# Optimization experiments

Hardware: AMD Instinct MI355X
Metric: run time of the kernel (lower is better)

Reference implementation:

```python
import jax, jax.numpy as jnp
import numpy as np

DIM, HID, BATCH = 64, 512, 8192


def setup_inputs() -> dict:
    key = jax.random.key(0)
    ks = jax.random.split(key, 6)
    s1 = 1.0 / np.sqrt(DIM + 1)
    s2 = 1.0 / np.sqrt(HID)
    return {
        "t": jax.random.uniform(ks[0], (1,), dtype=jnp.float32),
        "x": jax.random.normal(ks[1], (BATCH, DIM), dtype=jnp.float32),
        "W1": jax.random.normal(ks[2], (DIM + 1, HID), dtype=jnp.float32) * s1,
        "b1": jnp.zeros((HID,), jnp.float32),
        "W2": jax.random.normal(ks[3], (HID, HID), dtype=jnp.float32) * s2,
        "b2": jnp.zeros((HID,), jnp.float32),
        "W3": jax.random.normal(ks[4], (HID, DIM), dtype=jnp.float32) * s2,
        "b3": jnp.zeros((DIM,), jnp.float32),
    }


def _vf_single(ts, xs, W1, b1, W2, b2, W3, b3):
    # xs: [dim], ts: scalar. Time concatenated as extra input feature.
    h = jnp.concatenate([xs, ts[None]])          # [dim+1]
    h = jnp.tanh(h @ W1 + b1)                    # [hid]
    h = jnp.tanh(h @ W2 + b2)                    # [hid]
    return h @ W3 + b3                           # [dim]


def reference(t, x, W1, b1, W2, b2, W3, b3):
    ts = t[0]
    vf = lambda xs: _vf_single(ts, xs, W1, b1, W2, b2, W3, b3)
    v = jax.vmap(vf)(x)                                   # [B, dim]
    # Exact divergence: trace of per-sample Jacobian dv/dx.
    # (Replaces the torch per-dim autograd.grad loop with one batched jacfwd.)
    J = jax.vmap(jax.jacfwd(vf))(x)                       # [B, dim, dim]
    div = jnp.trace(J, axis1=-2, axis2=-1)                # [B]
    return (v, -div[:, None])
```

## Files before the change

### kernel.cpp

```cpp
#include <hip/hip_runtime.h>

#define DIM 64
#define HID 512
#define BATCH 8192
#define MB 32
#define NTHR 512

typedef __attribute__((ext_vector_type(8))) short short8;
typedef __attribute__((ext_vector_type(4))) float f32x4;
typedef __attribute__((ext_vector_type(16))) float f32x16;
typedef float float4_ __attribute__((ext_vector_type(4)));

#define Z16 {0.f,0.f,0.f,0.f,0.f,0.f,0.f,0.f,0.f,0.f,0.f,0.f,0.f,0.f,0.f,0.f}

__device__ __forceinline__ unsigned short f2bf(float f) {
    union { float f; unsigned u; } v; v.f = f;
    return (unsigned short)((v.u + 0x7FFFu + ((v.u >> 16) & 1u)) >> 16);
}
__device__ __forceinline__ float tanh_fast(float x) {
    float e = __expf(2.f * x);
    return 1.f - __fdividef(2.f, e + 1.f);
}

__global__ __launch_bounds__(256) void prep(
        const float* __restrict__ t,  const float* __restrict__ W1,
        const float* __restrict__ b1, const float* __restrict__ W2,
        const float* __restrict__ W3,
        unsigned short* __restrict__ w2pk, unsigned short* __restrict__ ppk,
        unsigned short* __restrict__ w3pk, unsigned short* __restrict__ w1pk,
        float* __restrict__ c1) {
    int b = blockIdx.x;
    if (b >= 288) {
        int n = (b - 288) * 256 + threadIdx.x;
        c1[n] = fmaf(t[0], W1[DIM * HID + n], b1[n]);
        return;
    }
    int gid = b * 256 + threadIdx.x;
    int f = gid >> 6, l = gid & 63;
    if (f < 512) {
        int nt = f >> 5, ks = f & 31;
        int n = nt * 32 + (l & 31), k0 = ks * 16 + (l >> 5) * 8;
        unsigned short* o = w2pk + (size_t)(f * 64 + l) * 8;
#pragma unroll
        for (int e = 0; e < 8; ++e) o[e] = f2bf(W2[(size_t)(k0 + e) * HID + n]);
    } else if (f < 1024) {
        int fi = f - 512;
        int nt = fi >> 5, ks = fi & 31;
        int n = nt * 32 + (l & 31), k0 = ks * 16 + (l >> 5) * 8;
        float m[8] = {0.f,0.f,0.f,0.f,0.f,0.f,0.f,0.f};
        for (int i = 0; i < DIM; ++i) {
            float w3 = W3[(size_t)n * DIM + i];
#pragma unroll
            for (int e = 0; e < 8; ++e) m[e] = fmaf(W1[(size_t)i * HID + k0 + e], w3, m[e]);
        }
        unsigned short* o = ppk + (size_t)(fi * 64 + l) * 8;
#pragma unroll
        for (int e = 0; e < 8; ++e) o[e] = f2bf(W2[(size_t)(k0 + e) * HID + n] * m[e]);
    } else if (f < 1088) {
        int fi = f - 1024;
        int nt = fi >> 4, ks = fi & 15;
        int n = nt * 16 + (l & 15), k0 = ks * 32 + (l >> 4) * 8;
        unsigned short* o = w3pk + (size_t)(fi * 64 + l) * 8;
#pragma unroll
        for (int e = 0; e < 8; ++e) o[e] = f2bf(W3[(size_t)(k0 + e) * DIM + n]);
    } else {
        int fi = f - 1088;
        int nt = fi >> 1, ks = fi & 1;
        int n = nt * 16 + (l & 15), k0 = ks * 32 + (l >> 4) * 8;
        unsigned short* o = w1pk + (size_t)(fi * 64 + l) * 8;
#pragma unroll
        for (int e = 0; e < 8; ++e) o[e] = f2bf(W1[(size_t)(k0 + e) * HID + n]);
    }
}

__device__ __forceinline__ int lds_addr(int row, int k) {
    return (row * 1024 + k * 2) ^ ((row & 7) << 4);
}

__global__ __launch_bounds__(NTHR, 2) void fused_main(
        const float* __restrict__ x,  const float* __restrict__ c1,
        const float* __restrict__ b2, const float* __restrict__ b3,
        const unsigned short* __restrict__ w1pk, const unsigned short* __restrict__ w2pk,
        const unsigned short* __restrict__ ppk,  const unsigned short* __restrict__ w3pk,
        float* __restrict__ out) {
    __shared__ unsigned short h1s[MB * HID];
    __shared__ unsigned short d1s[MB * HID];
    __shared__ unsigned short h2s[MB * HID];
    __shared__ float wred[8][MB];

    const int tid = threadIdx.x;
    const int w = tid >> 6;
    const int l = tid & 63;
    const int lr = l & 15, g = l >> 4;
    const int wm = w & 1, wn = w >> 1;
    const int s0 = blockIdx.x * MB;
    char* h1b = (char*)h1s; char* d1b = (char*)d1s; char* h2b = (char*)h2s;

    union U8 { short8 s8; unsigned short u[8]; };
    short8 ax[2];
#pragma unroll
    for (int ks = 0; ks < 2; ++ks) {
        const float* xp = x + (size_t)(s0 + wm * 16 + lr) * DIM + ks * 32 + g * 8;
        float4_ x0 = *(const float4_*)xp;
        float4_ x1 = *(const float4_*)(xp + 4);
        U8 u;
        u.u[0] = f2bf(x0.x); u.u[1] = f2bf(x0.y); u.u[2] = f2bf(x0.z); u.u[3] = f2bf(x0.w);
        u.u[4] = f2bf(x1.x); u.u[5] = f2bf(x1.y); u.u[6] = f2bf(x1.z); u.u[7] = f2bf(x1.w);
        ax[ks] = u.s8;
    }
    {
        f32x4 acc1[8];
#pragma unroll
        for (int nt = 0; nt < 8; ++nt) {
            const short8* bw = (const short8*)w1pk + (size_t)((wn * 8 + nt) * 2) * 64 + l;
            f32x4 a = {0.f, 0.f, 0.f, 0.f};
            a = __builtin_amdgcn_mfma_f32_16x16x32_bf16(ax[0], bw[0],  a, 0, 0, 0);
            a = __builtin_amdgcn_mfma_f32_16x16x32_bf16(ax[1], bw[64], a, 0, 0, 0);
            acc1[nt] = a;
        }
#pragma unroll
        for (int nt = 0; nt < 8; ++nt) {
            int c = (wn * 8 + nt) * 16 + lr;
            float c1v = c1[c];
#pragma unroll
            for (int r = 0; r < 4; ++r) {
                int row = wm * 16 + g * 4 + r;
                float h = tanh_fast(acc1[nt][r] + c1v);
                int a0 = lds_addr(row, c);
                *(unsigned short*)(h1b + a0) = f2bf(h);
                *(unsigned short*)(d1b + a0) = f2bf(fmaf(-h, h, 1.f));
            }
        }
    }
    __syncthreads();

    const int nt0 = w * 2, nt1 = w * 2 + 1;
    f32x16 z0 = Z16, z1 = Z16, sv0 = Z16, sv1 = Z16;
#pragma unroll 4
    for (int ks = 0; ks < 32; ++ks) {
        int arow = l & 31;
        int ab = lds_addr(arow, ks * 16 + (l >> 5) * 8);
        short8 ah = *(const short8*)(h1b + ab);
        short8 ad = *(const short8*)(d1b + ab);
        const short8* bw = (const short8*)w2pk;
        const short8* bp = (const short8*)ppk;
        short8 bw0 = bw[(size_t)(nt0 * 32 + ks) * 64 + l];
        short8 bw1 = bw[(size_t)(nt1 * 32 + ks) * 64 + l];
        short8 bp0 = bp[(size_t)(nt0 * 32 + ks) * 64 + l];
        short8 bp1 = bp[(size_t)(nt1 * 32 + ks) * 64 + l];
        z0  = __builtin_amdgcn_mfma_f32_32x32x16_bf16(ah, bw0, z0, 0, 0, 0);
        z1  = __builtin_amdgcn_mfma_f32_32x32x16_bf16(ah, bw1, z1, 0, 0, 0);
        sv0 = __builtin_amdgcn_mfma_f32_32x32x16_bf16(ad, bp0, sv0, 0, 0, 0);
        sv1 = __builtin_amdgcn_mfma_f32_32x32x16_bf16(ad, bp1, sv1, 0, 0, 0);
    }

    float divp[16];
#pragma unroll
    for (int r = 0; r < 16; ++r) divp[r] = 0.f;
#pragma unroll
    for (int j = 0; j < 2; ++j) {
        f32x16 z  = j ? z1 : z0;
        f32x16 sv = j ? sv1 : sv0;
        int c = (w * 2 + j) * 32 + (l & 31);
        float b2v = b2[c];
#pragma unroll
        for (int r = 0; r < 16; ++r) {
            int row = (r & 3) + 8 * (r >> 2) + 4 * (l >> 5);
            float h2 = tanh_fast(z[r] + b2v);
            float d2 = fmaf(-h2, h2, 1.f);
            divp[r] = fmaf(sv[r], d2, divp[r]);
            *(unsigned short*)(h2b + lds_addr(row, c)) = f2bf(h2);
        }
    }

#pragma unroll
    for (int off = 1; off < 32; off <<= 1) {
#pragma unroll
        for (int r = 0; r < 16; ++r) divp[r] += __shfl_xor(divp[r], off, 64);
    }
    if ((l & 31) == 0) {
#pragma unroll
        for (int r = 0; r < 16; ++r) {
            int row = (r & 3) + 8 * (r >> 2) + 4 * (l >> 5);
            wred[w][row] = divp[r];
        }
    }
    __syncthreads();
    if (tid < MB) {
        float d = 0.f;
#pragma unroll
        for (int ww = 0; ww < 8; ++ww) d += wred[ww][tid];
        out[(size_t)BATCH * DIM + s0 + tid] = -d;
    }

    {
        f32x4 acc = {0.f, 0.f, 0.f, 0.f};
        const short8* bw = (const short8*)w3pk + (size_t)(wn * 16) * 64 + l;
#pragma unroll
        for (int ks = 0; ks < 16; ++ks) {
            int ab = lds_addr(wm * 16 + lr, ks * 32 + g * 8);
            short8 a2 = *(const short8*)(h2b + ab);
            acc = __builtin_amdgcn_mfma_f32_16x16x32_bf16(a2, bw[ks * 64], acc, 0, 0, 0);
        }
        int c = wn * 16 + lr;
        float b3v = b3[c];
#pragma unroll
        for (int r = 0; r < 4; ++r)
            out[(size_t)(s0 + wm * 16 + g * 4 + r) * DIM + c] = acc[r] + b3v;
    }
}

extern "C" void kernel_launch(void* const* d_in, const int* in_sizes, int n_in,
                              void* d_out, int out_size, void* d_ws, size_t ws_size,
                              hipStream_t stream) {
    const float* t  = (const float*)d_in[0];
    const float* x  = (const float*)d_in[1];
    const float* W1 = (const float*)d_in[2];
    const float* b1 = (const float*)d_in[3];
    const float* W2 = (const float*)d_in[4];
    const float* b2 = (const float*)d_in[5];
    const float* W3 = (const float*)d_in[6];
    const float* b3 = (const float*)d_in[7];
    float* out = (float*)d_out;

    char* ws = (char*)d_ws;
    unsigned short* w2pk = (unsigned short*)ws;
    unsigned short* ppk  = (unsigned short*)(ws + (512 << 10));
    unsigned short* w3pk = (unsigned short*)(ws + (1 << 20));
    unsigned short* w1pk = (unsigned short*)(ws + (1 << 20) + (64 << 10));
    float*          c1   = (float*)(ws + (1 << 20) + (128 << 10));

    prep<<<290, 256, 0, stream>>>(t, W1, b1, W2, W3, w2pk, ppk, w3pk, w1pk, c1);
    fused_main<<<BATCH / MB, NTHR, 0, stream>>>(x, c1, b2, b3, w1pk, w2pk, ppk, w3pk, out);
}
```

Before: 36.95 us.

## Split hidden dimension across block pairs with 64-sample tiles and atomic output accumulation

Each block now processes 64 samples and half of the layer-2 output columns, so the grid doubles and each block streams half of the W2 and P weights. Warps are split into two roles, one computing the W2 product and one the divergence product, and layer-3 partial sums and divergence are combined across the two halves with float atomics into a pre-zeroed output. Prep is adjusted to stage W3 in shared memory and to repack W3 by half. This adds a memset, atomic traffic, larger shared-memory use and a heavier prep block, in exchange for reusing weight loads across more samples.

```diff
diff --git a/kernel.cpp b/kernel.cpp
--- a/kernel.cpp
+++ b/kernel.cpp
@@ -3,19 +3,27 @@
 #define DIM 64
 #define HID 512
 #define BATCH 8192
-#define MB 32
+#define SPB 64
 #define NTHR 512
 
 typedef __attribute__((ext_vector_type(8))) short short8;
 typedef __attribute__((ext_vector_type(4))) float f32x4;
 typedef __attribute__((ext_vector_type(16))) float f32x16;
 typedef float float4_ __attribute__((ext_vector_type(4)));
+typedef unsigned long long ull;
 
 #define Z16 {0.f,0.f,0.f,0.f,0.f,0.f,0.f,0.f,0.f,0.f,0.f,0.f,0.f,0.f,0.f,0.f}
+
+union U8 { short8 s8; unsigned short u[8]; };
+union U4 { ull v; unsigned short u[4]; };
+union FB { unsigned u; float f; };
 
 __device__ __forceinline__ unsigned short f2bf(float f) {
     union { float f; unsigned u; } v; v.f = f;
     return (unsigned short)((v.u + 0x7FFFu + ((v.u >> 16) & 1u)) >> 16);
+}
+__device__ __forceinline__ float bf2f(unsigned short b) {
+    FB v; v.u = (unsigned)b << 16; return v.f;
 }
 __device__ __forceinline__ float tanh_fast(float x) {
     float e = __expf(2.f * x);
@@ -29,6 +37,7 @@
         unsigned short* __restrict__ w2pk, unsigned short* __restrict__ ppk,
         unsigned short* __restrict__ w3pk, unsigned short* __restrict__ w1pk,
         float* __restrict__ c1) {
+    __shared__ float w3sT[DIM * 513];
     int b = blockIdx.x;
     if (b >= 288) {
         int n = (b - 288) * 256 + threadIdx.x;
@@ -44,12 +53,17 @@
 #pragma unroll
         for (int e = 0; e < 8; ++e) o[e] = f2bf(W2[(size_t)(k0 + e) * HID + n]);
     } else if (f < 1024) {
+        for (int idx = threadIdx.x; idx < HID * DIM; idx += 256) {
+            int n = idx >> 6, i = idx & 63;
+            w3sT[i * 513 + n] = W3[idx];
+        }
+        __syncthreads();
         int fi = f - 512;
         int nt = fi >> 5, ks = fi & 31;
         int n = nt * 32 + (l & 31), k0 = ks * 16 + (l >> 5) * 8;
         float m[8] = {0.f,0.f,0.f,0.f,0.f,0.f,0.f,0.f};
         for (int i = 0; i < DIM; ++i) {
-            float w3 = W3[(size_t)n * DIM + i];
+            float w3 = w3sT[i * 513 + n];
 #pragma unroll
             for (int e = 0; e < 8; ++e) m[e] = fmaf(W1[(size_t)i * HID + k0 + e], w3, m[e]);
         }
@@ -58,8 +72,8 @@
         for (int e = 0; e < 8; ++e) o[e] = f2bf(W2[(size_t)(k0 + e) * HID + n] * m[e]);
     } else if (f < 1088) {
         int fi = f - 1024;
-        int nt = fi >> 4, ks = fi & 15;
-        int n = nt * 16 + (l & 15), k0 = ks * 32 + (l >> 4) * 8;
+        int half = fi >> 5, nt = (fi >> 3) & 3, ks = fi & 7;
+        int n = nt * 16 + (l & 15), k0 = half * 256 + ks * 32 + (l >> 4) * 8;
         unsigned short* o = w3pk + (size_t)(fi * 64 + l) * 8;
 #pragma unroll
         for (int e = 0; e < 8; ++e) o[e] = f2bf(W3[(size_t)(k0 + e) * DIM + n]);
@@ -73,140 +87,152 @@
     }
 }
 
-__device__ __forceinline__ int lds_addr(int row, int k) {
-    return (row * 1024 + k * 2) ^ ((row & 7) << 4);
-}
-
 __global__ __launch_bounds__(NTHR, 2) void fused_main(
         const float* __restrict__ x,  const float* __restrict__ c1,
         const float* __restrict__ b2, const float* __restrict__ b3,
         const unsigned short* __restrict__ w1pk, const unsigned short* __restrict__ w2pk,
         const unsigned short* __restrict__ ppk,  const unsigned short* __restrict__ w3pk,
         float* __restrict__ out) {
-    __shared__ unsigned short h1s[MB * HID];
-    __shared__ unsigned short d1s[MB * HID];
-    __shared__ unsigned short h2s[MB * HID];
-    __shared__ float wred[8][MB];
-
-    const int tid = threadIdx.x;
-    const int w = tid >> 6;
-    const int l = tid & 63;
+    __shared__ unsigned short h1s[SPB * HID];
+    __shared__ unsigned short d1s[SPB * HID];
+    char* h1b = (char*)h1s;
+    char* d1b = (char*)d1s;
+
+    const int tid = threadIdx.x, w = tid >> 6, l = tid & 63;
     const int lr = l & 15, g = l >> 4;
-    const int wm = w & 1, wn = w >> 1;
-    const int s0 = blockIdx.x * MB;
-    char* h1b = (char*)h1s; char* d1b = (char*)d1s; char* h2b = (char*)h2s;
-
-    union U8 { short8 s8; unsigned short u[8]; };
-    short8 ax[2];
-#pragma unroll
-    for (int ks = 0; ks < 2; ++ks) {
-        const float* xp = x + (size_t)(s0 + wm * 16 + lr) * DIM + ks * 32 + g * 8;
-        float4_ x0 = *(const float4_*)xp;
-        float4_ x1 = *(const float4_*)(xp + 4);
-        U8 u;
-        u.u[0] = f2bf(x0.x); u.u[1] = f2bf(x0.y); u.u[2] = f2bf(x0.z); u.u[3] = f2bf(x0.w);
-        u.u[4] = f2bf(x1.x); u.u[5] = f2bf(x1.y); u.u[6] = f2bf(x1.z); u.u[7] = f2bf(x1.w);
-        ax[ks] = u.s8;
-    }
-    {
-        f32x4 acc1[8];
-#pragma unroll
-        for (int nt = 0; nt < 8; ++nt) {
-            const short8* bw = (const short8*)w1pk + (size_t)((wn * 8 + nt) * 2) * 64 + l;
-            f32x4 a = {0.f, 0.f, 0.f, 0.f};
-            a = __builtin_amdgcn_mfma_f32_16x16x32_bf16(ax[0], bw[0],  a, 0, 0, 0);
-            a = __builtin_amdgcn_mfma_f32_16x16x32_bf16(ax[1], bw[64], a, 0, 0, 0);
-            acc1[nt] = a;
-        }
-#pragma unroll
-        for (int nt = 0; nt < 8; ++nt) {
-            int c = (wn * 8 + nt) * 16 + lr;
-            float c1v = c1[c];
+    const int s0   = (blockIdx.x >> 1) * SPB;
+    const int half = blockIdx.x & 1;
+
+    short8 xf[4][2];
+#pragma unroll
+    for (int nt = 0; nt < 4; ++nt)
+#pragma unroll
+        for (int ks = 0; ks < 2; ++ks) {
+            const float* xp = x + (size_t)(s0 + nt * 16 + lr) * DIM + ks * 32 + g * 8;
+            float4_ x0 = *(const float4_*)xp;
+            float4_ x1 = *(const float4_*)(xp + 4);
+            U8 u;
+            u.u[0]=f2bf(x0.x); u.u[1]=f2bf(x0.y); u.u[2]=f2bf(x0.z); u.u[3]=f2bf(x0.w);
+            u.u[4]=f2bf(x1.x); u.u[5]=f2bf(x1.y); u.u[6]=f2bf(x1.z); u.u[7]=f2bf(x1.w);
+            xf[nt][ks] = u.s8;
+        }
+#pragma unroll
+    for (int mi = 0; mi < 4; ++mi) {
+        int mt = w * 4 + mi;
+        short8 a0 = ((const short8*)w1pk)[(size_t)((mt * 2 + 0) * 64 + l)];
+        short8 a1 = ((const short8*)w1pk)[(size_t)((mt * 2 + 1) * 64 + l)];
+        float c1q[4];
+#pragma unroll
+        for (int r = 0; r < 4; ++r) c1q[r] = c1[mt * 16 + g * 4 + r];
+#pragma unroll
+        for (int nt = 0; nt < 4; ++nt) {
+            f32x4 acc = {0.f, 0.f, 0.f, 0.f};
+            acc = __builtin_amdgcn_mfma_f32_16x16x32_bf16(a0, xf[nt][0], acc, 0, 0, 0);
+            acc = __builtin_amdgcn_mfma_f32_16x16x32_bf16(a1, xf[nt][1], acc, 0, 0, 0);
+            int sample = nt * 16 + lr;
+            U4 hu, du;
 #pragma unroll
             for (int r = 0; r < 4; ++r) {
-                int row = wm * 16 + g * 4 + r;
-                float h = tanh_fast(acc1[nt][r] + c1v);
-                int a0 = lds_addr(row, c);
-                *(unsigned short*)(h1b + a0) = f2bf(h);
-                *(unsigned short*)(d1b + a0) = f2bf(fmaf(-h, h, 1.f));
+                float h = tanh_fast(acc[r] + c1q[r]);
+                hu.u[r] = f2bf(h);
+                du.u[r] = f2bf(fmaf(-h, h, 1.f));
             }
+            int ab = (sample * 1024 + (mt * 16 + g * 4) * 2) ^ ((sample & 15) << 4);
+            *(ull*)(h1b + ab) = hu.v;
+            *(ull*)(d1b + ab) = du.v;
         }
     }
     __syncthreads();
 
-    const int nt0 = w * 2, nt1 = w * 2 + 1;
-    f32x16 z0 = Z16, z1 = Z16, sv0 = Z16, sv1 = Z16;
+    const int role = w >> 2;
+    const int wp = w & 3;
+    const int mgA = half * 8 + wp * 2, mgB = mgA + 1;
+    const short8* Af = (const short8*)(role ? ppk : w2pk);
+    const char* Bb = role ? d1b : h1b;
+
+    f32x16 a00 = Z16, a01 = Z16, a10 = Z16, a11 = Z16;
 #pragma unroll 4
     for (int ks = 0; ks < 32; ++ks) {
-        int arow = l & 31;
-        int ab = lds_addr(arow, ks * 16 + (l >> 5) * 8);
-        short8 ah = *(const short8*)(h1b + ab);
-        short8 ad = *(const short8*)(d1b + ab);
-        const short8* bw = (const short8*)w2pk;
-        const short8* bp = (const short8*)ppk;
-        short8 bw0 = bw[(size_t)(nt0 * 32 + ks) * 64 + l];
-        short8 bw1 = bw[(size_t)(nt1 * 32 + ks) * 64 + l];
-        short8 bp0 = bp[(size_t)(nt0 * 32 + ks) * 64 + l];
-        short8 bp1 = bp[(size_t)(nt1 * 32 + ks) * 64 + l];
-        z0  = __builtin_amdgcn_mfma_f32_32x32x16_bf16(ah, bw0, z0, 0, 0, 0);
-        z1  = __builtin_amdgcn_mfma_f32_32x32x16_bf16(ah, bw1, z1, 0, 0, 0);
-        sv0 = __builtin_amdgcn_mfma_f32_32x32x16_bf16(ad, bp0, sv0, 0, 0, 0);
-        sv1 = __builtin_amdgcn_mfma_f32_32x32x16_bf16(ad, bp1, sv1, 0, 0, 0);
-    }
-
-    float divp[16];
-#pragma unroll
-    for (int r = 0; r < 16; ++r) divp[r] = 0.f;
-#pragma unroll
-    for (int j = 0; j < 2; ++j) {
-        f32x16 z  = j ? z1 : z0;
-        f32x16 sv = j ? sv1 : sv0;
-        int c = (w * 2 + j) * 32 + (l & 31);
-        float b2v = b2[c];
-#pragma unroll
-        for (int r = 0; r < 16; ++r) {
-            int row = (r & 3) + 8 * (r >> 2) + 4 * (l >> 5);
-            float h2 = tanh_fast(z[r] + b2v);
-            float d2 = fmaf(-h2, h2, 1.f);
-            divp[r] = fmaf(sv[r], d2, divp[r]);
-            *(unsigned short*)(h2b + lds_addr(row, c)) = f2bf(h2);
-        }
-    }
-
-#pragma unroll
-    for (int off = 1; off < 32; off <<= 1) {
-#pragma unroll
-        for (int r = 0; r < 16; ++r) divp[r] += __shfl_xor(divp[r], off, 64);
-    }
-    if ((l & 31) == 0) {
-#pragma unroll
-        for (int r = 0; r < 16; ++r) {
-            int row = (r & 3) + 8 * (r >> 2) + 4 * (l >> 5);
-            wred[w][row] = divp[r];
-        }
+        int cb = ks * 32 + (l >> 5) * 16;
+        int r0 = l & 31, r1 = 32 + (l & 31);
+        short8 b0  = *(const short8*)(Bb + ((r0 * 1024 + cb) ^ ((r0 & 15) << 4)));
+        short8 b1v = *(const short8*)(Bb + ((r1 * 1024 + cb) ^ ((r1 & 15) << 4)));
+        short8 aA = Af[(size_t)((mgA * 32 + ks) * 64 + l)];
+        short8 aB = Af[(size_t)((mgB * 32 + ks) * 64 + l)];
+        a00 = __builtin_amdgcn_mfma_f32_32x32x16_bf16(aA, b0,  a00, 0, 0, 0);
+        a01 = __builtin_amdgcn_mfma_f32_32x32x16_bf16(aA, b1v, a01, 0, 0, 0);
+        a10 = __builtin_amdgcn_mfma_f32_32x32x16_bf16(aB, b0,  a10, 0, 0, 0);
+        a11 = __builtin_amdgcn_mfma_f32_32x32x16_bf16(aB, b1v, a11, 0, 0, 0);
     }
     __syncthreads();
-    if (tid < MB) {
-        float d = 0.f;
-#pragma unroll
-        for (int ww = 0; ww < 8; ++ww) d += wred[ww][tid];
-        out[(size_t)BATCH * DIM + s0 + tid] = -d;
+
+    const int hh = l >> 5;
+    if (role == 0) {
+#define Z_EPI(ACC, J, N2) { \
+        int mloc = wp * 2 + (J); \
+        int cgbase = (half * 8 + mloc) * 32; \
+        int sample = (N2) * 32 + (l & 31); \
+        _Pragma("unroll") \
+        for (int q = 0; q < 4; ++q) { \
+            U4 hu; \
+            _Pragma("unroll") \
+            for (int r3 = 0; r3 < 4; ++r3) { \
+                int rm = r3 + 8 * q + 4 * hh; \
+                float h2 = tanh_fast((ACC)[q * 4 + r3] + b2[cgbase + rm]); \
+                hu.u[r3] = f2bf(h2); \
+            } \
+            int ab = (sample * 512 + (mloc * 32 + 8 * q + 4 * hh) * 2) ^ ((sample & 15) << 4); \
+            *(ull*)(d1b + ab) = hu.v; \
+        } }
+        Z_EPI(a00, 0, 0) Z_EPI(a01, 0, 1) Z_EPI(a10, 1, 0) Z_EPI(a11, 1, 1)
+#undef Z_EPI
+    }
+    __syncthreads();
+    if (role == 1) {
+        float ds0 = 0.f, ds1 = 0.f;
+#define S_EPI(ACC, J, N2, DS) { \
+        int mloc = wp * 2 + (J); \
+        int sample = (N2) * 32 + (l & 31); \
+        _Pragma("unroll") \
+        for (int q = 0; q < 4; ++q) { \
+            int ab = (sample * 512 + (mloc * 32 + 8 * q + 4 * hh) * 2) ^ ((sample & 15) << 4); \
+            U4 hu; hu.v = *(const ull*)(d1b + ab); \
+            _Pragma("unroll") \
+            for (int r3 = 0; r3 < 4; ++r3) { \
+                float h2 = bf2f(hu.u[r3]); \
+                DS = fmaf((ACC)[q * 4 + r3], fmaf(-h2, h2, 1.f), DS); \
+            } \
+        } }
+        S_EPI(a00, 0, 0, ds0) S_EPI(a01, 0, 1, ds1) S_EPI(a10, 1, 0, ds0) S_EPI(a11, 1, 1, ds1)
+#undef S_EPI
+        ds0 += __shfl_xor(ds0, 32, 64);
+        ds1 += __shfl_xor(ds1, 32, 64);
+        if (l < 32) {
+            atomicAdd(out + (size_t)BATCH * DIM + s0 + l,      -ds0);
+            atomicAdd(out + (size_t)BATCH * DIM + s0 + 32 + l, -ds1);
+        }
     }
 
     {
-        f32x4 acc = {0.f, 0.f, 0.f, 0.f};
-        const short8* bw = (const short8*)w3pk + (size_t)(wn * 16) * 64 + l;
-#pragma unroll
-        for (int ks = 0; ks < 16; ++ks) {
-            int ab = lds_addr(wm * 16 + lr, ks * 32 + g * 8);
-            short8 a2 = *(const short8*)(h2b + ab);
-            acc = __builtin_amdgcn_mfma_f32_16x16x32_bf16(a2, bw[ks * 64], acc, 0, 0, 0);
-        }
-        int c = wn * 16 + lr;
-        float b3v = b3[c];
-#pragma unroll
-        for (int r = 0; r < 4; ++r)
-            out[(size_t)(s0 + wm * 16 + g * 4 + r) * DIM + c] = acc[r] + b3v;
+        const int mt3 = w >> 1, ntp = (w & 1) * 2;
+#pragma unroll
+        for (int jj = 0; jj < 2; ++jj) {
+            int nt = ntp + jj;
+            f32x4 acc3 = {0.f, 0.f, 0.f, 0.f};
+            const short8* W3f = (const short8*)w3pk + (size_t)((half * 32 + nt * 8) * 64 + l);
+#pragma unroll
+            for (int ks = 0; ks < 8; ++ks) {
+                int row = mt3 * 16 + lr;
+                int ab = (row * 512 + ks * 64 + g * 16) ^ ((row & 15) << 4);
+                short8 ah = *(const short8*)(d1b + ab);
+                acc3 = __builtin_amdgcn_mfma_f32_16x16x32_bf16(ah, W3f[ks * 64], acc3, 0, 0, 0);
+            }
+            float bv = half ? 0.f : b3[nt * 16 + lr];
+#pragma unroll
+            for (int r = 0; r < 4; ++r)
+                atomicAdd(out + (size_t)(s0 + mt3 * 16 + g * 4 + r) * DIM + nt * 16 + lr,
+                          acc3[r] + bv);
+        }
     }
 }
 
@@ -230,6 +256,7 @@
     unsigned short* w1pk = (unsigned short*)(ws + (1 << 20) + (64 << 10));
     float*          c1   = (float*)(ws + (1 << 20) + (128 << 10));
 
+    hipMemsetAsync(d_out, 0, (size_t)out_size * sizeof(float), stream);
     prep<<<290, 256, 0, stream>>>(t, W1, b1, W2, W3, w2pk, ppk, w3pk, w1pk, c1);
-    fused_main<<<BATCH / MB, NTHR, 0, stream>>>(x, c1, b2, b3, w1pk, w2pk, ppk, w3pk, out);
-}
+    fused_main<<<(BATCH / SPB) * 2, NTHR, 0, stream>>>(x, c1, b2, b3, w1pk, w2pk, ppk, w3pk, out);
+}
```

After: 45.79 us. +23.9%, slower.

## Use 1024-thread blocks with transposed layer-1 MFMA and prefetched layer-2 weights

Applied to the files above, without the earlier changes.

Doubles the block to 16 waves so each wave computes one 32-column tile of the hidden layer instead of two. Layer 1 is recomputed as W1^T times x^T, so each lane writes 4 contiguous bf16 values as one 64-bit LDS store, and the LDS swizzle is widened. The layer-2 loop software-prefetches the next weight fragments. The prep kernel now stages W3 in shared memory for the P-matrix build. The costs are the lost two-blocks-per-CU launch bound and half the waves sitting idle during the layer-3 matmul.

```diff
diff --git a/kernel.cpp b/kernel.cpp
--- a/kernel.cpp
+++ b/kernel.cpp
@@ -4,14 +4,18 @@
 #define HID 512
 #define BATCH 8192
 #define MB 32
-#define NTHR 512
+#define NTHR 1024
 
 typedef __attribute__((ext_vector_type(8))) short short8;
 typedef __attribute__((ext_vector_type(4))) float f32x4;
 typedef __attribute__((ext_vector_type(16))) float f32x16;
 typedef float float4_ __attribute__((ext_vector_type(4)));
+typedef unsigned long long ull;
 
 #define Z16 {0.f,0.f,0.f,0.f,0.f,0.f,0.f,0.f,0.f,0.f,0.f,0.f,0.f,0.f,0.f,0.f}
+
+union U8 { short8 s8; unsigned short u[8]; };
+union U4 { ull v; unsigned short u[4]; };
 
 __device__ __forceinline__ unsigned short f2bf(float f) {
     union { float f; unsigned u; } v; v.f = f;
@@ -29,6 +33,7 @@
         unsigned short* __restrict__ w2pk, unsigned short* __restrict__ ppk,
         unsigned short* __restrict__ w3pk, unsigned short* __restrict__ w1pk,
         float* __restrict__ c1) {
+    __shared__ float w3sT[DIM * 33];
     int b = blockIdx.x;
     if (b >= 288) {
         int n = (b - 288) * 256 + threadIdx.x;
@@ -44,12 +49,19 @@
 #pragma unroll
         for (int e = 0; e < 8; ++e) o[e] = f2bf(W2[(size_t)(k0 + e) * HID + n]);
     } else if (f < 1024) {
+        int ntb = (b * 4 - 512) >> 5;
+        for (int idx = threadIdx.x; idx < 32 * DIM; idx += 256) {
+            int dn = idx >> 6, i = idx & 63;
+            w3sT[i * 33 + dn] = W3[(size_t)(ntb * 32 + dn) * DIM + i];
+        }
+        __syncthreads();
         int fi = f - 512;
-        int nt = fi >> 5, ks = fi & 31;
-        int n = nt * 32 + (l & 31), k0 = ks * 16 + (l >> 5) * 8;
+        int ks = fi & 31;
+        int dn = l & 31, k0 = ks * 16 + (l >> 5) * 8;
+        int n = ntb * 32 + dn;
         float m[8] = {0.f,0.f,0.f,0.f,0.f,0.f,0.f,0.f};
         for (int i = 0; i < DIM; ++i) {
-            float w3 = W3[(size_t)n * DIM + i];
+            float w3 = w3sT[i * 33 + dn];
 #pragma unroll
             for (int e = 0; e < 8; ++e) m[e] = fmaf(W1[(size_t)i * HID + k0 + e], w3, m[e]);
         }
@@ -73,11 +85,11 @@
     }
 }
 
-__device__ __forceinline__ int lds_addr(int row, int k) {
-    return (row * 1024 + k * 2) ^ ((row & 7) << 4);
-}
-
-__global__ __launch_bounds__(NTHR, 2) void fused_main(
+__device__ __forceinline__ int act_addr(int sample, int colbyte) {
+    return (sample * 1024 + colbyte) ^ ((sample & 15) << 4);
+}
+
+__global__ __launch_bounds__(NTHR) void fused_main(
         const float* __restrict__ x,  const float* __restrict__ c1,
         const float* __restrict__ b2, const float* __restrict__ b3,
         const unsigned short* __restrict__ w1pk, const unsigned short* __restrict__ w2pk,
@@ -86,93 +98,83 @@
     __shared__ unsigned short h1s[MB * HID];
     __shared__ unsigned short d1s[MB * HID];
     __shared__ unsigned short h2s[MB * HID];
-    __shared__ float wred[8][MB];
-
-    const int tid = threadIdx.x;
-    const int w = tid >> 6;
-    const int l = tid & 63;
+    __shared__ float wred[16][MB];
+    char* h1b = (char*)h1s; char* d1b = (char*)d1s; char* h2b = (char*)h2s;
+
+    const int tid = threadIdx.x, w = tid >> 6, l = tid & 63;
     const int lr = l & 15, g = l >> 4;
-    const int wm = w & 1, wn = w >> 1;
     const int s0 = blockIdx.x * MB;
-    char* h1b = (char*)h1s; char* d1b = (char*)d1s; char* h2b = (char*)h2s;
-
-    union U8 { short8 s8; unsigned short u[8]; };
-    short8 ax[2];
-#pragma unroll
-    for (int ks = 0; ks < 2; ++ks) {
-        const float* xp = x + (size_t)(s0 + wm * 16 + lr) * DIM + ks * 32 + g * 8;
-        float4_ x0 = *(const float4_*)xp;
-        float4_ x1 = *(const float4_*)(xp + 4);
-        U8 u;
-        u.u[0] = f2bf(x0.x); u.u[1] = f2bf(x0.y); u.u[2] = f2bf(x0.z); u.u[3] = f2bf(x0.w);
-        u.u[4] = f2bf(x1.x); u.u[5] = f2bf(x1.y); u.u[6] = f2bf(x1.z); u.u[7] = f2bf(x1.w);
-        ax[ks] = u.s8;
-    }
-    {
-        f32x4 acc1[8];
-#pragma unroll
-        for (int nt = 0; nt < 8; ++nt) {
-            const short8* bw = (const short8*)w1pk + (size_t)((wn * 8 + nt) * 2) * 64 + l;
-            f32x4 a = {0.f, 0.f, 0.f, 0.f};
-            a = __builtin_amdgcn_mfma_f32_16x16x32_bf16(ax[0], bw[0],  a, 0, 0, 0);
-            a = __builtin_amdgcn_mfma_f32_16x16x32_bf16(ax[1], bw[64], a, 0, 0, 0);
-            acc1[nt] = a;
-        }
-#pragma unroll
-        for (int nt = 0; nt < 8; ++nt) {
-            int c = (wn * 8 + nt) * 16 + lr;
-            float c1v = c1[c];
+
+    short8 xf[2][2];
+#pragma unroll
+    for (int nt = 0; nt < 2; ++nt)
+#pragma unroll
+        for (int ks = 0; ks < 2; ++ks) {
+            const float* xp = x + (size_t)(s0 + nt * 16 + lr) * DIM + ks * 32 + g * 8;
+            float4_ x0 = *(const float4_*)xp;
+            float4_ x1 = *(const float4_*)(xp + 4);
+            U8 u;
+            u.u[0]=f2bf(x0.x); u.u[1]=f2bf(x0.y); u.u[2]=f2bf(x0.z); u.u[3]=f2bf(x0.w);
+            u.u[4]=f2bf(x1.x); u.u[5]=f2bf(x1.y); u.u[6]=f2bf(x1.z); u.u[7]=f2bf(x1.w);
+            xf[nt][ks] = u.s8;
+        }
+#pragma unroll
+    for (int mi = 0; mi < 2; ++mi) {
+        int mt = w * 2 + mi;
+        short8 a0 = ((const short8*)w1pk)[(size_t)((mt * 2 + 0) * 64 + l)];
+        short8 a1 = ((const short8*)w1pk)[(size_t)((mt * 2 + 1) * 64 + l)];
+        float c1q[4];
+#pragma unroll
+        for (int r = 0; r < 4; ++r) c1q[r] = c1[mt * 16 + g * 4 + r];
+#pragma unroll
+        for (int nt = 0; nt < 2; ++nt) {
+            f32x4 acc = {0.f, 0.f, 0.f, 0.f};
+            acc = __builtin_amdgcn_mfma_f32_16x16x32_bf16(a0, xf[nt][0], acc, 0, 0, 0);
+            acc = __builtin_amdgcn_mfma_f32_16x16x32_bf16(a1, xf[nt][1], acc, 0, 0, 0);
+            int sample = nt * 16 + lr;
+            U4 hu, du;
 #pragma unroll
             for (int r = 0; r < 4; ++r) {
-                int row = wm * 16 + g * 4 + r;
-                float h = tanh_fast(acc1[nt][r] + c1v);
-                int a0 = lds_addr(row, c);
-                *(unsigned short*)(h1b + a0) = f2bf(h);
-                *(unsigned short*)(d1b + a0) = f2bf(fmaf(-h, h, 1.f));
+                float h = tanh_fast(acc[r] + c1q[r]);
+                hu.u[r] = f2bf(h);
+                du.u[r] = f2bf(fmaf(-h, h, 1.f));
             }
+            int ab = act_addr(sample, (mt * 16 + g * 4) * 2);
+            *(ull*)(h1b + ab) = hu.v;
+            *(ull*)(d1b + ab) = du.v;
         }
     }
     __syncthreads();
 
-    const int nt0 = w * 2, nt1 = w * 2 + 1;
-    f32x16 z0 = Z16, z1 = Z16, sv0 = Z16, sv1 = Z16;
-#pragma unroll 4
+    const short8* bw = (const short8*)w2pk + (size_t)(w * 32) * 64 + l;
+    const short8* bp = (const short8*)ppk  + (size_t)(w * 32) * 64 + l;
+    f32x16 z = Z16, s = Z16;
+    short8 bwc = bw[0], bpc = bp[0];
+#pragma unroll 8
     for (int ks = 0; ks < 32; ++ks) {
-        int arow = l & 31;
-        int ab = lds_addr(arow, ks * 16 + (l >> 5) * 8);
+        short8 bwn = bwc, bpn = bpc;
+        if (ks < 31) { bwn = bw[(ks + 1) * 64]; bpn = bp[(ks + 1) * 64]; }
+        int ab = act_addr(l & 31, ks * 32 + (l >> 5) * 16);
         short8 ah = *(const short8*)(h1b + ab);
         short8 ad = *(const short8*)(d1b + ab);
-        const short8* bw = (const short8*)w2pk;
-        const short8* bp = (const short8*)ppk;
-        short8 bw0 = bw[(size_t)(nt0 * 32 + ks) * 64 + l];
-        short8 bw1 = bw[(size_t)(nt1 * 32 + ks) * 64 + l];
-        short8 bp0 = bp[(size_t)(nt0 * 32 + ks) * 64 + l];
-        short8 bp1 = bp[(size_t)(nt1 * 32 + ks) * 64 + l];
-        z0  = __builtin_amdgcn_mfma_f32_32x32x16_bf16(ah, bw0, z0, 0, 0, 0);
-        z1  = __builtin_amdgcn_mfma_f32_32x32x16_bf16(ah, bw1, z1, 0, 0, 0);
-        sv0 = __builtin_amdgcn_mfma_f32_32x32x16_bf16(ad, bp0, sv0, 0, 0, 0);
-        sv1 = __builtin_amdgcn_mfma_f32_32x32x16_bf16(ad, bp1, sv1, 0, 0, 0);
+        z = __builtin_amdgcn_mfma_f32_32x32x16_bf16(ah, bwc, z, 0, 0, 0);
+        s = __builtin_amdgcn_mfma_f32_32x32x16_bf16(ad, bpc, s, 0, 0, 0);
+        bwc = bwn; bpc = bpn;
     }
 
     float divp[16];
-#pragma unroll
-    for (int r = 0; r < 16; ++r) divp[r] = 0.f;
-#pragma unroll
-    for (int j = 0; j < 2; ++j) {
-        f32x16 z  = j ? z1 : z0;
-        f32x16 sv = j ? sv1 : sv0;
-        int c = (w * 2 + j) * 32 + (l & 31);
+    {
+        int c = w * 32 + (l & 31);
         float b2v = b2[c];
 #pragma unroll
         for (int r = 0; r < 16; ++r) {
             int row = (r & 3) + 8 * (r >> 2) + 4 * (l >> 5);
             float h2 = tanh_fast(z[r] + b2v);
             float d2 = fmaf(-h2, h2, 1.f);
-            divp[r] = fmaf(sv[r], d2, divp[r]);
-            *(unsigned short*)(h2b + lds_addr(row, c)) = f2bf(h2);
-        }
-    }
-
+            divp[r] = s[r] * d2;
+            *(unsigned short*)(h2b + act_addr(row, c * 2)) = f2bf(h2);
+        }
+    }
 #pragma unroll
     for (int off = 1; off < 32; off <<= 1) {
 #pragma unroll
@@ -189,24 +191,25 @@
     if (tid < MB) {
         float d = 0.f;
 #pragma unroll
-        for (int ww = 0; ww < 8; ++ww) d += wred[ww][tid];
+        for (int ww = 0; ww < 16; ++ww) d += wred[ww][tid];
         out[(size_t)BATCH * DIM + s0 + tid] = -d;
     }
 
-    {
+    if (w < 8) {
+        const int wm3 = w & 1, wn3 = w >> 1;
         f32x4 acc = {0.f, 0.f, 0.f, 0.f};
-        const short8* bw = (const short8*)w3pk + (size_t)(wn * 16) * 64 + l;
+        const short8* W3f = (const short8*)w3pk + (size_t)(wn3 * 16) * 64 + l;
 #pragma unroll
         for (int ks = 0; ks < 16; ++ks) {
-            int ab = lds_addr(wm * 16 + lr, ks * 32 + g * 8);
-            short8 a2 = *(const short8*)(h2b + ab);
-            acc = __builtin_amdgcn_mfma_f32_16x16x32_bf16(a2, bw[ks * 64], acc, 0, 0, 0);
-        }
-        int c = wn * 16 + lr;
+            int ab = act_addr(wm3 * 16 + lr, ks * 64 + g * 16);
+            short8 ah = *(const short8*)(h2b + ab);
+            acc = __builtin_amdgcn_mfma_f32_16x16x32_bf16(ah, W3f[ks * 64], acc, 0, 0, 0);
+        }
+        int c = wn3 * 16 + lr;
         float b3v = b3[c];
 #pragma unroll
         for (int r = 0; r < 4; ++r)
-            out[(size_t)(s0 + wm * 16 + g * 4 + r) * DIM + c] = acc[r] + b3v;
+            out[(size_t)(s0 + wm3 * 16 + g * 4 + r) * DIM + c] = acc[r] + b3v;
     }
 }
 
```

Result: faster. 35.21 us (-4.7%).
